# Kernel tuning notes

Hardware: AMD Instinct MI355X
Metric: run time of the kernel (lower is better)

The kernel has to match this reference:

```python
import jax, jax.numpy as jnp
import numpy as np

B, S, D, H, SKG = 4, 1024, 1024, 16, 256
HD = D // H  # head dim = 64


def setup_inputs() -> dict:
    key = jax.random.key(0)
    ks = jax.random.split(key, 8)
    std = 0.02
    return {
        "x": jax.random.normal(ks[0], (B, S, D), dtype=jnp.float32),
        "pred_kg": jax.random.normal(ks[1], (B, SKG, D), dtype=jnp.float32),
        "Wc": jax.random.normal(ks[2], (D, 3 * D), dtype=jnp.float32) * std,  # c_attn weight
        "bc": jnp.zeros((3 * D,), dtype=jnp.float32),
        "Wk": jax.random.normal(ks[3], (D, 2 * D), dtype=jnp.float32) * std,  # k_attn weight
        "bk": jnp.zeros((2 * D,), dtype=jnp.float32),
        "Wp": jax.random.normal(ks[4], (D, D), dtype=jnp.float32) * std,     # c_proj weight (shared)
        "bp": jnp.zeros((D,), dtype=jnp.float32),
    }


def _split_heads(t):  # [B, T, D] -> [B, H, T, HD]
    Bb, T, _ = t.shape
    return t.reshape(Bb, T, H, HD).transpose(0, 2, 1, 3)


def _merge_heads(t):  # [B, H, T, HD] -> [B, T, D]
    Bb, _, T, _ = t.shape
    return t.transpose(0, 2, 1, 3).reshape(Bb, T, D)


def reference(x, pred_kg, Wc, bc, Wk, bk, Wp, bp):
    # ---- self-attention branch (GPT-2 style, explicit causal bias blend) ----
    qkv = x @ Wc + bc                       # Conv1D: [B,S,3D]
    q, k, v = jnp.split(qkv, 3, axis=-1)
    q = _split_heads(q)                     # [B,H,S,HD]
    k = _split_heads(k)
    v = _split_heads(v)

    inv_sqrt_d = 1.0 / jnp.sqrt(jnp.float32(HD))
    w = jnp.einsum("bhqd,bhkd->bhqk", q, k) * inv_sqrt_d  # [B,H,S,S]
    causal = jnp.tril(jnp.ones((S, S), dtype=w.dtype))    # bias buffer slice b
    # faithful to: w = w * b - 10000.0 * (1 - b)
    w = w * causal - 10000.0 * (1.0 - causal)
    w = jax.nn.softmax(w, axis=-1)
    a = jnp.einsum("bhqk,bhkd->bhqd", w, v)
    a = _merge_heads(a) @ Wp + bp           # c_proj; resid dropout is identity in eval

    # ---- KG cross-attention branch (shares query and c_proj) ----
    kkv = pred_kg @ Wk + bk                 # [B,SKG,2D]
    kk, kv = jnp.split(kkv, 2, axis=-1)
    kk = _split_heads(kk)                   # [B,H,SKG,HD]
    kv = _split_heads(kv)
    w2 = jnp.einsum("bhqd,bhkd->bhqk", q, kk) * inv_sqrt_d  # [B,H,S,SKG]
    w2 = jax.nn.softmax(w2, axis=-1)
    ka = jnp.einsum("bhqk,bhkd->bhqd", w2, kv)
    ka = _merge_heads(ka) @ Wp + bp

    # concat the two branch outputs along the sequence axis: [B, S+SKG, D]
    return jnp.concatenate([a, ka], axis=1)
```

## Files before the change

### kernel.cpp

```cpp
#include <hip/hip_runtime.h>
#include <hip/hip_bf16.h>

typedef __bf16 bf16_t;
typedef bf16_t bf16x8 __attribute__((ext_vector_type(8)));
typedef bf16_t bf16x4 __attribute__((ext_vector_type(4)));
typedef float f32x4 __attribute__((ext_vector_type(4)));
typedef float f32x16 __attribute__((ext_vector_type(16)));

#define EXP2C 0.1803368867f
#define FEXP2(x) __builtin_amdgcn_exp2f(x)

__device__ __forceinline__ void gload16(const void* g, void* l) {
  __builtin_amdgcn_global_load_lds(
      (const __attribute__((address_space(1))) void*)g,
      (__attribute__((address_space(3))) void*)l, 16, 0, 0);
}

__device__ __forceinline__ unsigned pkbf(float lo, float hi) {
  unsigned short a = __builtin_bit_cast(unsigned short, (bf16_t)lo);
  unsigned short b = __builtin_bit_cast(unsigned short, (bf16_t)hi);
  return (unsigned)a | ((unsigned)b << 16);
}

__device__ __forceinline__ void plswap(unsigned& a, unsigned& b) {
#if __has_builtin(__builtin_amdgcn_permlane32_swap)
  auto r = __builtin_amdgcn_permlane32_swap(a, b, false, false);
  a = r[0]; b = r[1];
#else
  asm("v_permlane32_swap_b32 %0, %1" : "+v"(a), "+v"(b));
#endif
}
__device__ __forceinline__ float xmax32(float x) {
  unsigned a = __builtin_bit_cast(unsigned, x), b = a;
  plswap(a, b);
  return fmaxf(__builtin_bit_cast(float, a), __builtin_bit_cast(float, b));
}
__device__ __forceinline__ float xsum32(float x) {
  unsigned a = __builtin_bit_cast(unsigned, x), b = a;
  plswap(a, b);
  return __builtin_bit_cast(float, a) + __builtin_bit_cast(float, b);
}

__global__ __launch_bounds__(256) void prep_kernel(
    const float* __restrict__ x, bf16_t* __restrict__ xb,
    const float* __restrict__ pkg, bf16_t* __restrict__ pkb,
    const float* __restrict__ Wc, bf16_t* __restrict__ Wct,
    const float* __restrict__ Wk, bf16_t* __restrict__ Wkt,
    const float* __restrict__ Wp, bf16_t* __restrict__ Wpt) {
  __shared__ float tile[32][33];
  const int bid = blockIdx.x, tid = threadIdx.x;
  if (bid < 5120) {
    int i = bid * 256 + tid;
    const float* src; bf16_t* dst;
    if (i < 1048576) { src = x; dst = xb; }
    else { i -= 1048576; src = pkg; dst = pkb; }
    float4 v = reinterpret_cast<const float4*>(src)[i];
    bf16x4 o = { (bf16_t)v.x, (bf16_t)v.y, (bf16_t)v.z, (bf16_t)v.w };
    reinterpret_cast<bf16x4*>(dst)[i] = o;
    return;
  }
  int r = bid - 5120;
  int xx = r % 192, ky = r / 192;
  const float* W; bf16_t* T; int N;
  if (xx < 96) { W = Wc; T = Wct; N = 3072; }
  else if (xx < 160) { W = Wk; T = Wkt; N = 2048; xx -= 96; }
  else { W = Wp; T = Wpt; N = 1024; xx -= 160; }
  const int K = 1024;
  int tx = tid & 31, ty = tid >> 5;
  int n0 = xx * 32, k0 = ky * 32;
#pragma unroll
  for (int i = 0; i < 4; ++i)
    tile[ty + i * 8][tx] = W[(size_t)(k0 + ty + i * 8) * N + n0 + tx];
  __syncthreads();
#pragma unroll
  for (int i = 0; i < 4; ++i)
    T[(size_t)(n0 + ty + i * 8) * K + k0 + tx] = (bf16_t)tile[tx][ty + i * 8];
}

__global__ __launch_bounds__(256) void pack2_kernel(
    const bf16_t* __restrict__ src0, bf16_t* __restrict__ kd0, bf16_t* __restrict__ vd0,
    const bf16_t* __restrict__ src1, bf16_t* __restrict__ kd1, bf16_t* __restrict__ vd1) {
  __shared__ bf16_t vt[32][72];
  const int tid = threadIdx.x;
  int x = blockIdx.x;
  const int bh = blockIdx.y;
  const bf16_t* src; bf16_t *kd, *vd; int R, stride, kcol, vcol, NT, t;
  if (x < 32) { src = src0; kd = kd0; vd = vd0; R = 1024; stride = 3072; kcol = 1024; vcol = 2048; NT = 32; t = x; }
  else        { src = src1; kd = kd1; vd = vd1; R = 256;  stride = 2048; kcol = 0;    vcol = 1024; NT = 8;  t = x - 32; }
  const int b = bh >> 4, h = bh & 15;
  const size_t srow = (size_t)b * R + t * 32;
  const size_t obase = ((size_t)bh * NT + t) * 2048;
  {
    int r = tid >> 3, c = tid & 7;
    bf16x8 d = *(const bf16x8*)&src[(srow + r) * stride + vcol + h * 64 + c * 8];
    *(bf16x8*)&vt[r][c * 8] = d;
  }
  {
    int ks = tid >> 6, l = tid & 63;
    int hi8 = (l >> 5) * 8;
    bf16x8 d = *(const bf16x8*)&src[(srow + (l & 31)) * stride + kcol + h * 64 + ks * 16 + hi8];
    *(bf16x8*)&kd[obase + ks * 512 + l * 8] = d;
  }
  __syncthreads();
  {
    int dd = tid >> 6, l = tid & 63;
    int mb = dd >> 1, ks = dd & 1;
    int hd = mb * 32 + (l & 31);
    int kvr = ks * 16 + (l >> 5) * 8;
    bf16x8 o;
#pragma unroll
    for (int j = 0; j < 8; ++j) o[j] = vt[kvr + j][hd];
    *(bf16x8*)&vd[obase + dd * 512 + l * 8] = o;
  }
}

#define GBAR() __builtin_amdgcn_s_barrier()
#define LGKM0() asm volatile("s_waitcnt lgkmcnt(0)" ::: "memory")

__device__ __forceinline__ void gemm256_body(
    char* smem, const bf16_t* __restrict__ A, const bf16_t* __restrict__ Bt,
    const float* __restrict__ bias, bf16_t* __restrict__ Cout,
    int N, int K, int bx, int by) {
  const int tid = threadIdx.x;
  const int l = tid & 63, w = tid >> 6;
  const int lr = l & 15, lg = l >> 4;
  const int m0 = by * 256, n0 = bx * 256;
  const int wr = (w >> 2) * 128, wc = (w & 3) * 64;
  const int hA = w >> 2, hB = (w >> 1) & 1;

  const int sr = tid >> 3;
  const int scb = ((tid & 7) * 16) ^ ((sr & 7) << 4);
  const bf16_t* Ab = A + (size_t)m0 * K + (scb >> 1);
  const bf16_t* Bb = Bt + (size_t)n0 * K + (scb >> 1);
  const int nk = K >> 6;
  const int xr = (lr & 7) << 4;

  auto STAGE_A = [&](int t, int h) {
    const bf16_t* g = Ab + (size_t)(h * 128 + sr) * K + t * 64;
    char* d = smem + ((size_t)(t & 1) * 2 + h) * 16384 + tid * 16;
    gload16(g, d);
    gload16(g + (size_t)64 * K, d + 8192);
  };
  auto STAGE_B = [&](int t, int h) {
    const bf16_t* g = Bb + (size_t)(h * 128 + sr) * K + t * 64;
    char* d = smem + 65536 + ((size_t)(t & 1) * 2 + h) * 16384 + tid * 16;
    gload16(g, d);
    gload16(g + (size_t)64 * K, d + 8192);
  };

  f32x4 acc[8][4] = {};
  bf16x8 af[4][2], bf[2][2][2];

  STAGE_A(0, 0); STAGE_A(0, 1); STAGE_B(0, 0); STAGE_B(0, 1);
  asm volatile("s_waitcnt vmcnt(0)" ::: "memory");
  GBAR();

  for (int t = 0; t < nk; ++t) {
    const char* pA = smem + ((size_t)(t & 1) * 2 + hA) * 16384;
    const char* pB = smem + 65536 + ((size_t)(t & 1) * 2 + hB) * 16384;
    auto LDA = [&](int mf, int ks) {
      return *(const bf16x8*)(pA + (mf * 16 + lr) * 128 + ((ks * 64 + lg * 16) ^ xr));
    };
    auto LDB = [&](int nf, int ks) {
      return *(const bf16x8*)(pB + ((w & 1) * 64 + nf * 16 + lr) * 128 + ((ks * 64 + lg * 16) ^ xr));
    };
#pragma unroll
    for (int mf = 0; mf < 4; ++mf) { af[mf][0] = LDA(mf, 0); af[mf][1] = LDA(mf, 1); }
#pragma unroll
    for (int nf = 0; nf < 2; ++nf) { bf[0][nf][0] = LDB(nf, 0); bf[0][nf][1] = LDB(nf, 1); }
    if (t + 1 < nk) { STAGE_A(t + 1, 0); STAGE_B(t + 1, 0); }
    GBAR(); LGKM0();
    __builtin_amdgcn_s_setprio(1);
#pragma unroll
    for (int mf = 0; mf < 4; ++mf)
#pragma unroll
      for (int nf = 0; nf < 2; ++nf) {
        acc[mf][nf] = __builtin_amdgcn_mfma_f32_16x16x32_bf16(af[mf][0], bf[0][nf][0], acc[mf][nf], 0, 0, 0);
        acc[mf][nf] = __builtin_amdgcn_mfma_f32_16x16x32_bf16(af[mf][1], bf[0][nf][1], acc[mf][nf], 0, 0, 0);
      }
    __builtin_amdgcn_s_setprio(0);
    GBAR();
#pragma unroll
    for (int nf = 0; nf < 2; ++nf) { bf[1][nf][0] = LDB(2 + nf, 0); bf[1][nf][1] = LDB(2 + nf, 1); }
    if (t + 1 < nk) { STAGE_A(t + 1, 1); STAGE_B(t + 1, 1); }
    GBAR(); LGKM0();
    __builtin_amdgcn_s_setprio(1);
#pragma unroll
    for (int mf = 0; mf < 4; ++mf)
#pragma unroll
      for (int nf = 0; nf < 2; ++nf) {
        acc[mf][2 + nf] = __builtin_amdgcn_mfma_f32_16x16x32_bf16(af[mf][0], bf[1][nf][0], acc[mf][2 + nf], 0, 0, 0);
        acc[mf][2 + nf] = __builtin_amdgcn_mfma_f32_16x16x32_bf16(af[mf][1], bf[1][nf][1], acc[mf][2 + nf], 0, 0, 0);
      }
    __builtin_amdgcn_s_setprio(0);
    GBAR();
#pragma unroll
    for (int mf = 0; mf < 4; ++mf) { af[mf][0] = LDA(4 + mf, 0); af[mf][1] = LDA(4 + mf, 1); }
    GBAR(); LGKM0();
    __builtin_amdgcn_s_setprio(1);
#pragma unroll
    for (int mf = 0; mf < 4; ++mf)
#pragma unroll
      for (int nf = 0; nf < 2; ++nf) {
        acc[4 + mf][nf] = __builtin_amdgcn_mfma_f32_16x16x32_bf16(af[mf][0], bf[0][nf][0], acc[4 + mf][nf], 0, 0, 0);
        acc[4 + mf][nf] = __builtin_amdgcn_mfma_f32_16x16x32_bf16(af[mf][1], bf[0][nf][1], acc[4 + mf][nf], 0, 0, 0);
      }
    __builtin_amdgcn_s_setprio(0);
    GBAR();
    __builtin_amdgcn_s_setprio(1);
#pragma unroll
    for (int mf = 0; mf < 4; ++mf)
#pragma unroll
      for (int nf = 0; nf < 2; ++nf) {
        acc[4 + mf][2 + nf] = __builtin_amdgcn_mfma_f32_16x16x32_bf16(af[mf][0], bf[1][nf][0], acc[4 + mf][2 + nf], 0, 0, 0);
        acc[4 + mf][2 + nf] = __builtin_amdgcn_mfma_f32_16x16x32_bf16(af[mf][1], bf[1][nf][1], acc[4 + mf][2 + nf], 0, 0, 0);
      }
    __builtin_amdgcn_s_setprio(0);
    asm volatile("s_waitcnt vmcnt(0)" ::: "memory");
    GBAR();
  }

#pragma unroll
  for (int mf = 0; mf < 8; ++mf) {
#pragma unroll
    for (int nf = 0; nf < 4; ++nf) {
      int col = n0 + wc + nf * 16 + lr;
      float bb = bias[col];
      int rowb = m0 + wr + mf * 16 + lg * 4;
#pragma unroll
      for (int r = 0; r < 4; ++r) {
        float v = acc[mf][nf][r] + bb;
        ((bf16_t*)Cout)[(size_t)(rowb + r) * N + col] = (bf16_t)v;
      }
    }
  }
}

__global__ __launch_bounds__(512, 1) void gemm2_kernel(
    const bf16_t* __restrict__ A0, const bf16_t* __restrict__ B0,
    const float* __restrict__ bi0, bf16_t* __restrict__ C0,
    const bf16_t* __restrict__ A1, const bf16_t* __restrict__ B1,
    const float* __restrict__ bi1, bf16_t* __restrict__ C1) {
  extern __shared__ char smem[];
  int bid = blockIdx.x;
  int wg = (bid & 7) * 28 + (bid >> 3);
  if (wg < 192)
    gemm256_body(smem, A0, B0, bi0, C0, 3072, 1024, wg % 12, wg / 12);
  else {
    int r = wg - 192;
    gemm256_body(smem, A1, B1, bi1, C1, 2048, 1024, r % 8, r / 8);
  }
}

#define MFMA2(mi, ni)                                                         \
  acc[mi][ni] = __builtin_amdgcn_mfma_f32_16x16x32_bf16(af[(mi) & 1][0], bf[ni][0], acc[mi][ni], 0, 0, 0); \
  acc[mi][ni] = __builtin_amdgcn_mfma_f32_16x16x32_bf16(af[(mi) & 1][1], bf[ni][1], acc[mi][ni], 0, 0, 0);
#define MFMA8(qm, qn)                                                         \
  MFMA2(2 * (qm) + 0, 2 * (qn) + 0) MFMA2(2 * (qm) + 0, 2 * (qn) + 1)         \
  MFMA2(2 * (qm) + 1, 2 * (qn) + 0) MFMA2(2 * (qm) + 1, 2 * (qn) + 1)

template <int OUTF32>
__device__ __forceinline__ void gemm8_body(
    char* smem, const bf16_t* __restrict__ A, const bf16_t* __restrict__ Bt,
    const float* __restrict__ bias, void* __restrict__ Cout,
    int N, int K, int bx, int by) {
  const int tid = threadIdx.x;
  const int l = tid & 63, w = tid >> 6;
  const int lr = l & 15, lg = l >> 4;
  const int m0 = by * 256, n0 = bx * 128;
  const int wr = (w >> 1) * 64, wc = (w & 1) * 64;

  const int sr = tid >> 3;
  const int scb = ((tid & 7) * 16) ^ ((sr & 7) << 4);
  const bf16_t* Ab = A + (size_t)m0 * K + (scb >> 1);
  const bf16_t* Bb = Bt + (size_t)n0 * K + (scb >> 1);
  const int nk = K >> 6;

  const int hA = w >> 2;
  const int rA = ((w >> 1) & 1) * 64 + lr;
  const int rB = wc + lr;
  const int xr = (lr & 7) << 4;

  auto STAGE_A = [&](int t, int h) {
    const bf16_t* g = Ab + (size_t)(h * 128 + sr) * K + t * 64;
    char* d = smem + ((size_t)(t & 1) * 2 + h) * 16384 + tid * 16;
    gload16(g, d);
    gload16(g + (size_t)64 * K, d + 8192);
  };
  auto STAGE_B = [&](int t) {
    const bf16_t* g = Bb + (size_t)sr * K + t * 64;
    char* d = smem + 65536 + (size_t)(t & 1) * 16384 + tid * 16;
    gload16(g, d);
    gload16(g + (size_t)64 * K, d + 8192);
  };

  f32x4 acc[4][4] = {};
  bf16x8 af[2][2], bf[4][2];

  STAGE_A(0, 0); STAGE_A(0, 1); STAGE_B(0); STAGE_B(1); STAGE_A(1, 0);
  asm volatile("s_waitcnt vmcnt(4)" ::: "memory");
  GBAR();

  for (int t = 0; t < nk; ++t) {
    const char* pA = smem + ((size_t)(t & 1) * 2 + hA) * 16384;
    const char* pB = smem + 65536 + (size_t)(t & 1) * 16384;
    auto LDA = [&](int mf, int ks) {
      return *(const bf16x8*)(pA + (rA + mf * 16) * 128 + ((ks * 64 + lg * 16) ^ xr));
    };
    auto LDB = [&](int nf, int ks) {
      return *(const bf16x8*)(pB + (rB + nf * 16) * 128 + ((ks * 64 + lg * 16) ^ xr));
    };
    af[0][0] = LDA(0, 0); af[0][1] = LDA(0, 1);
    af[1][0] = LDA(1, 0); af[1][1] = LDA(1, 1);
    bf[0][0] = LDB(0, 0); bf[0][1] = LDB(0, 1);
    bf[1][0] = LDB(1, 0); bf[1][1] = LDB(1, 1);
    if (t + 1 < nk) STAGE_A(t + 1, 1);
    GBAR(); LGKM0();
    __builtin_amdgcn_s_setprio(1);
    MFMA8(0, 0)
    __builtin_amdgcn_s_setprio(0);
    GBAR();
    bf[2][0] = LDB(2, 0); bf[2][1] = LDB(2, 1);
    bf[3][0] = LDB(3, 0); bf[3][1] = LDB(3, 1);
    GBAR(); LGKM0();
    __builtin_amdgcn_s_setprio(1);
    MFMA8(0, 1)
    __builtin_amdgcn_s_setprio(0);
    GBAR();
    af[0][0] = LDA(2, 0); af[0][1] = LDA(2, 1);
    af[1][0] = LDA(3, 0); af[1][1] = LDA(3, 1);
    if (t + 2 < nk) STAGE_B(t + 2);
    GBAR(); LGKM0();
    __builtin_amdgcn_s_setprio(1);
    MFMA8(1, 0)
    __builtin_amdgcn_s_setprio(0);
    GBAR();
    if (t + 2 < nk) STAGE_A(t + 2, 0);
    GBAR();
    __builtin_amdgcn_s_setprio(1);
    MFMA8(1, 1)
    __builtin_amdgcn_s_setprio(0);
    if (t + 2 < nk)      asm volatile("s_waitcnt vmcnt(4)" ::: "memory");
    else if (t + 1 < nk) asm volatile("s_waitcnt vmcnt(0)" ::: "memory");
    GBAR();
  }

#pragma unroll
  for (int mf = 0; mf < 4; ++mf) {
#pragma unroll
    for (int nf = 0; nf < 4; ++nf) {
      int col = n0 + wc + nf * 16 + lr;
      float bb = bias[col];
      int rowb = m0 + wr + mf * 16 + lg * 4;
#pragma unroll
      for (int r = 0; r < 4; ++r) {
        float v = acc[mf][nf][r] + bb;
        if constexpr (OUTF32)
          ((float*)Cout)[(size_t)(rowb + r) * N + col] = v;
        else
          ((bf16_t*)Cout)[(size_t)(rowb + r) * N + col] = (bf16_t)v;
      }
    }
  }
}

__global__ __launch_bounds__(512, 1) void gemm_proj_kernel(
    const bf16_t* __restrict__ A, const bf16_t* __restrict__ Bt,
    const float* __restrict__ bias, float* __restrict__ Cout) {
  extern __shared__ char smem[];
  int bid = blockIdx.x;
  int wg = (bid & 7) * 32 + (bid >> 3);
  gemm8_body<1>(smem, A, Bt, bias, Cout, 1024, 1024, wg % 8, wg / 8);
}

#define STAGE(bf, t)                                                         \
  {                                                                          \
    gload16(kba + (size_t)(t) * 2048 + tid * 8, &sKV[bf][tid * 16]);         \
    gload16(vba + (size_t)(t) * 2048 + tid * 8, &sKV[bf][4096 + tid * 16]);  \
  }
#define QKT()                                                                \
  {                                                                          \
    __builtin_amdgcn_s_setprio(1);                                           \
    _Pragma("unroll") for (int ks = 0; ks < 4; ++ks)                         \
        sa = __builtin_amdgcn_mfma_f32_32x32x16_bf16(kf[ks], qf[ks], sa, 0, 0, 0); \
    __builtin_amdgcn_s_setprio(0);                                           \
  }
#define SMPV(vf, tcur)                                                       \
  {                                                                          \
    float sv[16];                                                            \
    const bool mt = is_self && ((tcur) == qw);                               \
    _Pragma("unroll") for (int r = 0; r < 16; ++r) {                         \
      float v = sa[r];                                                       \
      if (mt) {                                                              \
        int kvr = (r & 3) + 8 * (r >> 2) + kv4;                              \
        v = (kvr > ql) ? -1e30f : v;                                         \
      }                                                                      \
      sv[r] = v;                                                             \
    }                                                                        \
    float tm = fmaxf(                                                        \
        fmaxf(fmaxf(fmaxf(sv[0], sv[1]), fmaxf(sv[2], sv[3])),               \
              fmaxf(fmaxf(sv[4], sv[5]), fmaxf(sv[6], sv[7]))),              \
        fmaxf(fmaxf(fmaxf(sv[8], sv[9]), fmaxf(sv[10], sv[11])),             \
              fmaxf(fmaxf(sv[12], sv[13]), fmaxf(sv[14], sv[15]))));         \
    tm = xmax32(tm);                                                         \
    if (!__all(tm <= mcur + 64.f)) {                                         \
      float mn = fmaxf(mcur, tm);                                            \
      float sc = FEXP2((mcur - mn) * EXP2C);                                 \
      mcur = mn;                                                             \
      lcur *= sc;                                                            \
      _Pragma("unroll") for (int mb = 0; mb < 2; ++mb)                       \
          _Pragma("unroll") for (int r = 0; r < 16; ++r) oacc[mb][r] *= sc;  \
    }                                                                        \
    const float hm = mcur * EXP2C;                                           \
    float pf[16];                                                            \
    _Pragma("unroll") for (int r = 0; r < 16; ++r)                           \
        pf[r] = FEXP2(__builtin_fmaf(sv[r], EXP2C, -hm));                    \
    float ps = (((pf[0] + pf[1]) + (pf[2] + pf[3])) +                        \
                ((pf[4] + pf[5]) + (pf[6] + pf[7]))) +                       \
               (((pf[8] + pf[9]) + (pf[10] + pf[11])) +                      \
                ((pf[12] + pf[13]) + (pf[14] + pf[15])));                    \
    ps = xsum32(ps);                                                         \
    lcur += ps;                                                              \
    unsigned o01 = pkbf(pf[0], pf[1]), o23 = pkbf(pf[2], pf[3]);             \
    unsigned o45 = pkbf(pf[4], pf[5]), o67 = pkbf(pf[6], pf[7]);             \
    unsigned o89 = pkbf(pf[8], pf[9]), o1011 = pkbf(pf[10], pf[11]);         \
    unsigned o1213 = pkbf(pf[12], pf[13]), o1415 = pkbf(pf[14], pf[15]);     \
    plswap(o01, o45); plswap(o23, o67);                                      \
    plswap(o89, o1213); plswap(o1011, o1415);                                \
    uint4 w0 = { o01, o23, o45, o67 };                                       \
    uint4 w1 = { o89, o1011, o1213, o1415 };                                 \
    bf16x8 pb0 = __builtin_bit_cast(bf16x8, w0);                             \
    bf16x8 pb1 = __builtin_bit_cast(bf16x8, w1);                             \
    __builtin_amdgcn_s_setprio(1);                                           \
    oacc[0] = __builtin_amdgcn_mfma_f32_32x32x16_bf16(vf[0], pb0, oacc[0], 0, 0, 0); \
    oacc[0] = __builtin_amdgcn_mfma_f32_32x32x16_bf16(vf[1], pb1, oacc[0], 0, 0, 0); \
    oacc[1] = __builtin_amdgcn_mfma_f32_32x32x16_bf16(vf[2], pb0, oacc[1], 0, 0, 0); \
    oacc[1] = __builtin_amdgcn_mfma_f32_32x32x16_bf16(vf[3], pb1, oacc[1], 0, 0, 0); \
    __builtin_amdgcn_s_setprio(0);                                           \
  }

__global__ __launch_bounds__(256) void attn_kernel(
    const bf16_t* __restrict__ qkv,
    const bf16_t* __restrict__ kfs, const bf16_t* __restrict__ vfs,
    const bf16_t* __restrict__ kfc, const bf16_t* __restrict__ vfc,
    bf16_t* __restrict__ obuf) {
  __shared__ __align__(16) char sKV[3][8192];

  const int tid = threadIdx.x;
  const int w = tid >> 6, l = tid & 63;
  const int ql = l & 31;
  const bool uhi = l >= 32;
  const int kv4 = uhi ? 4 : 0;
  const int hi8 = uhi ? 8 : 0;

  const int bid = blockIdx.x;
  const bool is_self = bid < 512;
  int qb, bh, nt;
  if (is_self) {
    qb = 7 - (bid >> 6);
    bh = bid & 63;
    nt = qb * 4 + 4;
  } else {
    int cb = bid - 512;
    qb = cb >> 6;
    bh = cb & 63;
    nt = 8;
  }
  const int qw = qb * 4 + w;
  const int b = bh >> 4, h = bh & 15;
  const int hcol = h * 64;
  const int q0 = qw * 32;
  const int tlim = is_self ? qw : (nt - 1);

  const bf16_t* kba; const bf16_t* vba; int ooff;
  if (is_self) {
    kba = kfs + (size_t)bh * 32 * 2048; vba = vfs + (size_t)bh * 32 * 2048; ooff = 0;
  } else {
    kba = kfc + (size_t)bh * 8 * 2048;  vba = vfc + (size_t)bh * 8 * 2048;  ooff = 1024;
  }

  const bf16_t* qrow = qkv + (size_t)(b * 1024 + q0 + ql) * 3072 + hcol + hi8;
  bf16x8 qf[4];
#pragma unroll
  for (int ks = 0; ks < 4; ++ks) qf[ks] = *(const bf16x8*)(qrow + ks * 16);

  float mcur = -1e30f, lcur = 0.f;
  f32x16 oacc[2] = {};

  STAGE(0, 0); STAGE(1, 1);
  asm volatile("s_waitcnt vmcnt(2)" ::: "memory");
  __builtin_amdgcn_s_barrier();

  int cur = 0;
  for (int t = 0; t < nt; ++t) {
    int s2 = cur + 2; if (s2 >= 3) s2 -= 3;
    if (t + 2 < nt) STAGE(s2, t + 2);
    if (t <= tlim) {
      bf16x8 kf[4], vf[4];
#pragma unroll
      for (int c = 0; c < 4; ++c)
        kf[c] = *(const bf16x8*)&sKV[cur][c * 1024 + l * 16];
#pragma unroll
      for (int c = 0; c < 4; ++c)
        vf[c] = *(const bf16x8*)&sKV[cur][4096 + c * 1024 + l * 16];
      f32x16 sa = {};
      QKT();
      SMPV(vf, t);
    }
    if (t + 2 < nt)      asm volatile("s_waitcnt vmcnt(2)" ::: "memory");
    else if (t + 1 < nt) asm volatile("s_waitcnt vmcnt(0)" ::: "memory");
    __builtin_amdgcn_s_barrier();
    cur = cur + 1; if (cur >= 3) cur -= 3;
  }
  __syncthreads();

  const float rl = 1.0f / lcur;
  char* swp = &sKV[0][0] + w * 4096;
#pragma unroll
  for (int mb = 0; mb < 2; ++mb)
#pragma unroll
    for (int r2 = 0; r2 < 8; ++r2) {
      float lo = oacc[mb][2 * r2] * rl;
      float hiv = oacc[mb][2 * r2 + 1] * rl;
      int hdb = (r2 & 1) * 2 + 8 * (r2 >> 1) + kv4 + mb * 32;
      int off = (ql * 128 + hdb * 2) ^ ((ql & 7) << 4);
      *(unsigned*)(swp + off) = pkbf(lo, hiv);
    }
  __syncthreads();
  const int orow = b * 2048 + ooff + q0;
#pragma unroll
  for (int it = 0; it < 4; ++it) {
    int idx = it * 64 + l;
    int q = idx >> 3, ch = idx & 7;
    int off = (q * 128 + ch * 16) ^ ((q & 7) << 4);
    uint4 d = *(uint4*)(swp + off);
    *(uint4*)&obuf[(size_t)(orow + q) * 1024 + hcol + ch * 8] = d;
  }
}

extern "C" void kernel_launch(void* const* d_in, const int* in_sizes, int n_in,
                              void* d_out, int out_size, void* d_ws, size_t ws_size,
                              hipStream_t stream) {
  (void)in_sizes; (void)n_in; (void)out_size; (void)ws_size;
  const float* x   = (const float*)d_in[0];
  const float* pkg = (const float*)d_in[1];
  const float* Wc  = (const float*)d_in[2];
  const float* bc  = (const float*)d_in[3];
  const float* Wk  = (const float*)d_in[4];
  const float* bk  = (const float*)d_in[5];
  const float* Wp  = (const float*)d_in[6];
  const float* bp  = (const float*)d_in[7];
  float* out = (float*)d_out;

  char* ws = (char*)d_ws;
  const size_t MB = 1u << 20;
  bf16_t* xb   = (bf16_t*)(ws + 0 * MB);
  bf16_t* pkb  = (bf16_t*)(ws + 8 * MB);
  bf16_t* Wct  = (bf16_t*)(ws + 10 * MB);
  bf16_t* Wkt  = (bf16_t*)(ws + 16 * MB);
  bf16_t* Wpt  = (bf16_t*)(ws + 20 * MB);
  bf16_t* kkvb = (bf16_t*)(ws + 22 * MB);
  bf16_t* abuf = (bf16_t*)(ws + 26 * MB);
  bf16_t* vfs  = (bf16_t*)(ws + 0 * MB);
  bf16_t* kfc  = (bf16_t*)(ws + 8 * MB);
  bf16_t* vfc  = (bf16_t*)(ws + 10 * MB);
  bf16_t* qkvb = (bf16_t*)d_out;
  bf16_t* kfs  = (bf16_t*)((char*)d_out + 24 * MB);

  prep_kernel<<<11264, 256, 0, stream>>>(x, xb, pkg, pkb, Wc, Wct, Wk, Wkt, Wp, Wpt);
  gemm2_kernel<<<224, 512, 131072, stream>>>(xb, Wct, bc, qkvb, pkb, Wkt, bk, kkvb);
  pack2_kernel<<<dim3(40, 64), 256, 0, stream>>>(qkvb, kfs, vfs, kkvb, kfc, vfc);
  attn_kernel<<<1024, 256, 0, stream>>>(qkvb, kfs, vfs, kfc, vfc, abuf);
  gemm_proj_kernel<<<256, 512, 98304, stream>>>(abuf, Wpt, bp, out);
}
```

Before: 110.6 us.

## Double-buffer 64-row KV tiles in attention instead of triple-buffered 32-row tiles

The attention loop now stages two 32-row K/V tiles (64 KV rows) per iteration into a double-buffered 32 KB LDS area, replacing the triple-buffered single-tile scheme. Each iteration prefetches the next pair of tiles and runs two QK^T/softmax/PV steps, then synchronises. This halves the number of barriers per block. In exchange, prefetch depth drops from two tiles ahead to one iteration ahead, and __syncthreads waits for all outstanding loads, which may expose more load latency.

New measurement: 110.7 us, median of 2. Within noise of the previous version (+0.1%).

```diff
diff --git a/kernel.cpp b/kernel.cpp
--- a/kernel.cpp
+++ b/kernel.cpp
@@ -373,70 +373,77 @@
   gemm8_body<1>(smem, A, Bt, bias, Cout, 1024, 1024, wg % 8, wg / 8);
 }
 
-#define STAGE(bf, t)                                                         \
-  {                                                                          \
-    gload16(kba + (size_t)(t) * 2048 + tid * 8, &sKV[bf][tid * 16]);         \
-    gload16(vba + (size_t)(t) * 2048 + tid * 8, &sKV[bf][4096 + tid * 16]);  \
-  }
-#define QKT()                                                                \
-  {                                                                          \
-    __builtin_amdgcn_s_setprio(1);                                           \
-    _Pragma("unroll") for (int ks = 0; ks < 4; ++ks)                         \
+#define STAGE64(bf, it)                                                       \
+  {                                                                           \
+    gload16(kba + (size_t)(it) * 4096 + tid * 8, &sKV[bf][tid * 16]);         \
+    gload16(kba + (size_t)(it) * 4096 + 2048 + tid * 8, &sKV[bf][4096 + tid * 16]); \
+    gload16(vba + (size_t)(it) * 4096 + tid * 8, &sKV[bf][8192 + tid * 16]);  \
+    gload16(vba + (size_t)(it) * 4096 + 2048 + tid * 8, &sKV[bf][12288 + tid * 16]); \
+  }
+#define QKT(sub)                                                              \
+  {                                                                           \
+    _Pragma("unroll") for (int c = 0; c < 4; ++c)                             \
+        kf[c] = *(const bf16x8*)&sKV[buf][(sub) * 4096 + c * 1024 + l * 16];  \
+    sa = (f32x16){};                                                          \
+    __builtin_amdgcn_s_setprio(1);                                            \
+    _Pragma("unroll") for (int ks = 0; ks < 4; ++ks)                          \
         sa = __builtin_amdgcn_mfma_f32_32x32x16_bf16(kf[ks], qf[ks], sa, 0, 0, 0); \
-    __builtin_amdgcn_s_setprio(0);                                           \
-  }
-#define SMPV(vf, tcur)                                                       \
-  {                                                                          \
-    float sv[16];                                                            \
-    const bool mt = is_self && ((tcur) == qw);                               \
-    _Pragma("unroll") for (int r = 0; r < 16; ++r) {                         \
-      float v = sa[r];                                                       \
-      if (mt) {                                                              \
-        int kvr = (r & 3) + 8 * (r >> 2) + kv4;                              \
-        v = (kvr > ql) ? -1e30f : v;                                         \
-      }                                                                      \
-      sv[r] = v;                                                             \
-    }                                                                        \
-    float tm = fmaxf(                                                        \
-        fmaxf(fmaxf(fmaxf(sv[0], sv[1]), fmaxf(sv[2], sv[3])),               \
-              fmaxf(fmaxf(sv[4], sv[5]), fmaxf(sv[6], sv[7]))),              \
-        fmaxf(fmaxf(fmaxf(sv[8], sv[9]), fmaxf(sv[10], sv[11])),             \
-              fmaxf(fmaxf(sv[12], sv[13]), fmaxf(sv[14], sv[15]))));         \
-    tm = xmax32(tm);                                                         \
-    if (!__all(tm <= mcur + 64.f)) {                                         \
-      float mn = fmaxf(mcur, tm);                                            \
-      float sc = FEXP2((mcur - mn) * EXP2C);                                 \
-      mcur = mn;                                                             \
-      lcur *= sc;                                                            \
-      _Pragma("unroll") for (int mb = 0; mb < 2; ++mb)                       \
-          _Pragma("unroll") for (int r = 0; r < 16; ++r) oacc[mb][r] *= sc;  \
-    }                                                                        \
-    const float hm = mcur * EXP2C;                                           \
-    float pf[16];                                                            \
-    _Pragma("unroll") for (int r = 0; r < 16; ++r)                           \
-        pf[r] = FEXP2(__builtin_fmaf(sv[r], EXP2C, -hm));                    \
-    float ps = (((pf[0] + pf[1]) + (pf[2] + pf[3])) +                        \
-                ((pf[4] + pf[5]) + (pf[6] + pf[7]))) +                       \
-               (((pf[8] + pf[9]) + (pf[10] + pf[11])) +                      \
-                ((pf[12] + pf[13]) + (pf[14] + pf[15])));                    \
-    ps = xsum32(ps);                                                         \
-    lcur += ps;                                                              \
-    unsigned o01 = pkbf(pf[0], pf[1]), o23 = pkbf(pf[2], pf[3]);             \
-    unsigned o45 = pkbf(pf[4], pf[5]), o67 = pkbf(pf[6], pf[7]);             \
-    unsigned o89 = pkbf(pf[8], pf[9]), o1011 = pkbf(pf[10], pf[11]);         \
-    unsigned o1213 = pkbf(pf[12], pf[13]), o1415 = pkbf(pf[14], pf[15]);     \
-    plswap(o01, o45); plswap(o23, o67);                                      \
-    plswap(o89, o1213); plswap(o1011, o1415);                                \
-    uint4 w0 = { o01, o23, o45, o67 };                                       \
-    uint4 w1 = { o89, o1011, o1213, o1415 };                                 \
-    bf16x8 pb0 = __builtin_bit_cast(bf16x8, w0);                             \
-    bf16x8 pb1 = __builtin_bit_cast(bf16x8, w1);                             \
-    __builtin_amdgcn_s_setprio(1);                                           \
+    __builtin_amdgcn_s_setprio(0);                                            \
+  }
+#define SMPV(sub, tcur)                                                       \
+  {                                                                           \
+    _Pragma("unroll") for (int c = 0; c < 4; ++c)                             \
+        vf[c] = *(const bf16x8*)&sKV[buf][8192 + (sub) * 4096 + c * 1024 + l * 16]; \
+    float sv[16];                                                             \
+    const bool mt = is_self && ((tcur) == qw);                                \
+    _Pragma("unroll") for (int r = 0; r < 16; ++r) {                          \
+      float v = sa[r];                                                        \
+      if (mt) {                                                               \
+        int kvr = (r & 3) + 8 * (r >> 2) + kv4;                               \
+        v = (kvr > ql) ? -1e30f : v;                                          \
+      }                                                                       \
+      sv[r] = v;                                                              \
+    }                                                                         \
+    float tm = fmaxf(                                                         \
+        fmaxf(fmaxf(fmaxf(sv[0], sv[1]), fmaxf(sv[2], sv[3])),                \
+              fmaxf(fmaxf(sv[4], sv[5]), fmaxf(sv[6], sv[7]))),               \
+        fmaxf(fmaxf(fmaxf(sv[8], sv[9]), fmaxf(sv[10], sv[11])),              \
+              fmaxf(fmaxf(sv[12], sv[13]), fmaxf(sv[14], sv[15]))));          \
+    tm = xmax32(tm);                                                          \
+    if (!__all(tm <= mcur + 64.f)) {                                          \
+      float mn = fmaxf(mcur, tm);                                             \
+      float sc = FEXP2((mcur - mn) * EXP2C);                                  \
+      mcur = mn;                                                              \
+      lcur *= sc;                                                             \
+      _Pragma("unroll") for (int mb = 0; mb < 2; ++mb)                        \
+          _Pragma("unroll") for (int r = 0; r < 16; ++r) oacc[mb][r] *= sc;   \
+    }                                                                         \
+    const float hm = mcur * EXP2C;                                            \
+    float pf[16];                                                             \
+    _Pragma("unroll") for (int r = 0; r < 16; ++r)                            \
+        pf[r] = FEXP2(__builtin_fmaf(sv[r], EXP2C, -hm));                     \
+    float ps = (((pf[0] + pf[1]) + (pf[2] + pf[3])) +                         \
+                ((pf[4] + pf[5]) + (pf[6] + pf[7]))) +                        \
+               (((pf[8] + pf[9]) + (pf[10] + pf[11])) +                       \
+                ((pf[12] + pf[13]) + (pf[14] + pf[15])));                     \
+    ps = xsum32(ps);                                                          \
+    lcur += ps;                                                               \
+    unsigned o01 = pkbf(pf[0], pf[1]), o23 = pkbf(pf[2], pf[3]);              \
+    unsigned o45 = pkbf(pf[4], pf[5]), o67 = pkbf(pf[6], pf[7]);              \
+    unsigned o89 = pkbf(pf[8], pf[9]), o1011 = pkbf(pf[10], pf[11]);          \
+    unsigned o1213 = pkbf(pf[12], pf[13]), o1415 = pkbf(pf[14], pf[15]);      \
+    plswap(o01, o45); plswap(o23, o67);                                       \
+    plswap(o89, o1213); plswap(o1011, o1415);                                 \
+    uint4 w0 = { o01, o23, o45, o67 };                                        \
+    uint4 w1 = { o89, o1011, o1213, o1415 };                                  \
+    bf16x8 pb0 = __builtin_bit_cast(bf16x8, w0);                              \
+    bf16x8 pb1 = __builtin_bit_cast(bf16x8, w1);                              \
+    __builtin_amdgcn_s_setprio(1);                                            \
     oacc[0] = __builtin_amdgcn_mfma_f32_32x32x16_bf16(vf[0], pb0, oacc[0], 0, 0, 0); \
     oacc[0] = __builtin_amdgcn_mfma_f32_32x32x16_bf16(vf[1], pb1, oacc[0], 0, 0, 0); \
     oacc[1] = __builtin_amdgcn_mfma_f32_32x32x16_bf16(vf[2], pb0, oacc[1], 0, 0, 0); \
     oacc[1] = __builtin_amdgcn_mfma_f32_32x32x16_bf16(vf[3], pb1, oacc[1], 0, 0, 0); \
-    __builtin_amdgcn_s_setprio(0);                                           \
+    __builtin_amdgcn_s_setprio(0);                                            \
   }
 
 __global__ __launch_bounds__(256) void attn_kernel(
@@ -444,7 +451,7 @@
     const bf16_t* __restrict__ kfs, const bf16_t* __restrict__ vfs,
     const bf16_t* __restrict__ kfc, const bf16_t* __restrict__ vfc,
     bf16_t* __restrict__ obuf) {
-  __shared__ __align__(16) char sKV[3][8192];
+  __shared__ __align__(16) char sKV[2][16384];
 
   const int tid = threadIdx.x;
   const int w = tid >> 6, l = tid & 63;
@@ -455,22 +462,23 @@
 
   const int bid = blockIdx.x;
   const bool is_self = bid < 512;
-  int qb, bh, nt;
+  int qb, bh, nt32;
   if (is_self) {
     qb = 7 - (bid >> 6);
     bh = bid & 63;
-    nt = qb * 4 + 4;
+    nt32 = qb * 4 + 4;
   } else {
     int cb = bid - 512;
     qb = cb >> 6;
     bh = cb & 63;
-    nt = 8;
+    nt32 = 8;
   }
   const int qw = qb * 4 + w;
   const int b = bh >> 4, h = bh & 15;
   const int hcol = h * 64;
   const int q0 = qw * 32;
-  const int tlim = is_self ? qw : (nt - 1);
+  const int tlim = is_self ? qw : (nt32 - 1);
+  const int nit = nt32 >> 1;
 
   const bf16_t* kba; const bf16_t* vba; int ooff;
   if (is_self) {
@@ -486,33 +494,26 @@
 
   float mcur = -1e30f, lcur = 0.f;
   f32x16 oacc[2] = {};
-
-  STAGE(0, 0); STAGE(1, 1);
-  asm volatile("s_waitcnt vmcnt(2)" ::: "memory");
-  __builtin_amdgcn_s_barrier();
-
-  int cur = 0;
-  for (int t = 0; t < nt; ++t) {
-    int s2 = cur + 2; if (s2 >= 3) s2 -= 3;
-    if (t + 2 < nt) STAGE(s2, t + 2);
-    if (t <= tlim) {
-      bf16x8 kf[4], vf[4];
-#pragma unroll
-      for (int c = 0; c < 4; ++c)
-        kf[c] = *(const bf16x8*)&sKV[cur][c * 1024 + l * 16];
-#pragma unroll
-      for (int c = 0; c < 4; ++c)
-        vf[c] = *(const bf16x8*)&sKV[cur][4096 + c * 1024 + l * 16];
-      f32x16 sa = {};
-      QKT();
-      SMPV(vf, t);
+  f32x16 sa;
+  bf16x8 kf[4], vf[4];
+
+  STAGE64(0, 0);
+  __syncthreads();
+  int buf = 0;
+  for (int it = 0; it < nit; ++it) {
+    if (it + 1 < nit) STAGE64(buf ^ 1, it + 1);
+    const int t0 = 2 * it, t1 = 2 * it + 1;
+    if (t0 <= tlim) {
+      QKT(0);
+      SMPV(0, t0);
     }
-    if (t + 2 < nt)      asm volatile("s_waitcnt vmcnt(2)" ::: "memory");
-    else if (t + 1 < nt) asm volatile("s_waitcnt vmcnt(0)" ::: "memory");
-    __builtin_amdgcn_s_barrier();
-    cur = cur + 1; if (cur >= 3) cur -= 3;
-  }
-  __syncthreads();
+    if (t1 <= tlim) {
+      QKT(1);
+      SMPV(1, t1);
+    }
+    __syncthreads();
+    buf ^= 1;
+  }
 
   const float rl = 1.0f / lcur;
   char* swp = &sKV[0][0] + w * 4096;
```
